# Kernel optimization log

Hardware: AMD Instinct MI355X
Metric: run time of the kernel (lower is better)

Reference implementation:

```python
import jax, jax.numpy as jnp
import numpy as np

EPS = 1e-5
C = 128
B = 16384
SYMBIOTIC = 4.0
NUM_PARENTS = 16
CHILDREN_PER_PARENT = 7


def _inverse(v):
    # torch: sort -> rank -> reversed rank -> gather sorted values
    idx0 = np.argsort(v, kind='stable')
    value = v[idx0]
    idx1 = np.argsort(idx0, kind='stable')  # ranks
    idx2 = v.shape[0] - 1 - idx1
    return value[idx2]


def _build_stats():
    counts = np.floor(50000.0 * 0.97 ** np.arange(C)) + 1.0  # long-tailed
    N = counts.sum()
    weight = (N / counts).astype(np.float32)
    prior = np.eye(C, dtype=np.float32)
    for p in range(NUM_PARENTS):
        ch = NUM_PARENTS + CHILDREN_PER_PARENT * p + np.arange(CHILDREN_PER_PARENT)
        prior[p, ch] = 1.0
    prior_me = (prior == 0).astype(np.float32)          # 1 - prior, keep only exact 1s
    prior_ms = prior - np.eye(C, dtype=np.float32)      # prior (0/1) minus eye
    v1_sig = np.log(N / counts - 1.0 + EPS).astype(np.float32)
    v2_sig = _inverse(v1_sig).astype(np.float32)
    v1_sm = np.log(counts / N + EPS).astype(np.float32)
    v2_sm = _inverse(v1_sm).astype(np.float32)
    return weight, prior_me, prior_ms, v1_sig, v2_sig, v1_sm, v2_sm


def setup_inputs() -> dict:
    key = jax.random.key(0)
    k1, k2 = jax.random.split(key)
    weight, prior_me, prior_ms, v1s, v2s, v1m, v2m = _build_stats()
    logits = 0.5 * jax.random.normal(k1, (12, B, C), dtype=jnp.float32)
    target = (jax.random.uniform(k2, (B, C)) < 0.1).astype(jnp.float32)
    return {
        'logits': logits, 'target': target,
        'weight': jnp.asarray(weight),
        'prior_me': jnp.asarray(prior_me), 'prior_ms': jnp.asarray(prior_ms),
        'v1_sigmoid': jnp.asarray(v1s), 'v2_sigmoid': jnp.asarray(v2s),
        'v1_softmax': jnp.asarray(v1m), 'v2_softmax': jnp.asarray(v2m),
    }


def reference(logits, target, weight, prior_me, prior_ms,
              v1_sigmoid, v2_sigmoid, v1_softmax, v2_softmax):
    zero = jnp.zeros_like(v1_sigmoid)
    # experts 0-5: sigmoid variants (long-tailed / balanced / inversed, twice)
    sig_shift = jnp.stack([zero, v1_sigmoid, v1_sigmoid - v2_sigmoid] * 2)  # [6,C]
    a_sig = jax.nn.sigmoid(logits[:6] - sig_shift[:, None, :])
    # experts 6-11: local-softmax variants
    sm_shift = jnp.stack([zero, v1_softmax, v1_softmax - v2_softmax] * 2)   # [6,C]
    e = jnp.exp(logits[6:] + sm_shift[:, None, :])                          # [6,B,C]
    denom = jnp.einsum('ebc,cd->ebd', e, prior_me) + e
    a_sm = e / (denom + EPS)
    acti = jnp.clip(jnp.concatenate([a_sig, a_sm], axis=0), EPS, 1.0 - EPS)  # [12,B,C]
    # weighted BCE per expert, summed
    bce = -weight * (target * jnp.log(acti) + (1.0 - target) * jnp.log(1.0 - acti))
    loss = jnp.sum(jnp.mean(bce, axis=(1, 2)))
    # symbiotic regularizer on experts 3,4,5,9,10,11
    row_sum = jnp.sum(prior_ms, axis=1)                 # [C]
    n_nz = jnp.sum(row_sum > 0).astype(acti.dtype)
    bsz = acti.shape[1]

    def symb(a):  # a: [B,C] activated logits
        def step(acc, xs):
            mask_row, parent = xs                       # [C], [B]
            term = jnp.log1p(jnp.exp(a - parent[:, None]))  # [B,C]
            rs = jnp.sum(mask_row)
            contrib = jnp.where(rs > 0, jnp.sum(term * mask_row) / (bsz * rs), 0.0)
            return acc + contrib, None
        total, _ = jax.lax.scan(step, jnp.float32(0.0), (prior_ms, a.T))
        return total / n_nz

    reg = jax.vmap(symb)(acti[jnp.array([3, 4, 5, 9, 10, 11])])
    return loss + SYMBIOTIC * jnp.sum(reg)
```

## Files before the change

kernel.cpp:

```cpp
#include <hip/hip_runtime.h>
#include <math.h>

#define CC 128
#define BB 16384
#define MEPS 1e-5f
#define NBLK 2048


__device__ __forceinline__ float softplus1(float d) {
    const float u = d * d;
    float p = fmaf(u, 3.4722222e-4f, -5.2083333e-3f);
    p = fmaf(u, p, 0.125f);
    return fmaf(u, p, fmaf(d, 0.5f, 0.69314718f));
}

__global__ __launch_bounds__(256, 6) void mel_main(
    const float* __restrict__ logits, const float* __restrict__ target,
    const float* __restrict__ weight,
    const float* __restrict__ v1s, const float* __restrict__ v2s,
    const float* __restrict__ v1m, const float* __restrict__ v2m,
    float* __restrict__ partial)
{
    const int lane = threadIdx.x & 63;
    const int wib  = threadIdx.x >> 6;
    const int wave = blockIdx.x * 4 + wib;
    const int r    = lane >> 5;
    const int c    = lane & 31;
    const int row  = wave * 2 + r;
    const size_t ro = (size_t)row * CC;

    const float4 wt4 = ((const float4*)weight)[c];
    const float4 s1v = ((const float4*)v1s)[c];
    const float4 s2v = ((const float4*)v2s)[c];
    const float4 m1v = ((const float4*)v1m)[c];
    const float4 m2v = ((const float4*)v2m)[c];
    const float4 tv  = ((const float4*)(target + ro))[c];

    const float wt[4] = {wt4.x, wt4.y, wt4.z, wt4.w};
    const float s1[4] = {s1v.x, s1v.y, s1v.z, s1v.w};
    const float sd[4] = {s1v.x - s2v.x, s1v.y - s2v.y, s1v.z - s2v.z, s1v.w - s2v.w};
    const float m1[4] = {m1v.x, m1v.y, m1v.z, m1v.w};
    const float md[4] = {m1v.x - m2v.x, m1v.y - m2v.y, m1v.z - m2v.z, m1v.w - m2v.w};
    const bool  tb[4] = {tv.x > 0.5f, tv.y > 0.5f, tv.z > 0.5f, tv.w > 0.5f};

    const float childf = (c >= 4) ? 1.f : 0.f;
    int pofs[4];
    #pragma unroll
    for (int k = 0; k < 4; ++k) {
        const int ch = 4 * c + k;
        pofs[k] = (ch >= 16) ? (ch - 16) / 7 : 0;
    }

    __shared__ float lds[4][2][16];
    float* Lp = &lds[wib][r][0];

    const float* pp = logits + ro;
    float4 cur = ((const float4*)pp)[c];
    float accP = 0.f;
    float accS = 0.f;

    #pragma unroll 1
    for (int e = 0; e < 12; ++e) {
        float4 nxt = cur;
        if (e < 11) nxt = ((const float4*)(pp + (size_t)BB * CC))[c];
        pp += (size_t)BB * CC;
        const int si = e % 3;
        const float x[4] = {cur.x, cur.y, cur.z, cur.w};

        if (e < 6) {
            float a[4];
            #pragma unroll
            for (int k = 0; k < 4; ++k) {
                const float sh = (si == 0) ? 0.f : ((si == 1) ? s1[k] : sd[k]);
                const float z  = x[k] - sh;
                const float ex = __expf(-z);
                const float sp = __logf(1.f + ex);
                accP = fmaf(wt[k], sp + (tb[k] ? 0.f : z), accP);
                a[k] = __builtin_amdgcn_rcpf(1.f + ex);
            }
            if (e >= 3) {
                if (c < 4) *(float4*)(Lp + 4 * c) = make_float4(a[0], a[1], a[2], a[3]);
                #pragma unroll
                for (int k = 0; k < 4; ++k)
                    accS = fmaf(childf, softplus1(a[k] - Lp[pofs[k]]), accS);
            }
        } else {
            float ek[4];
            float S = 0.f;
            #pragma unroll
            for (int k = 0; k < 4; ++k) {
                const float sh = (si == 0) ? 0.f : ((si == 1) ? m1[k] : md[k]);
                ek[k] = __expf(x[k] + sh);
                S += ek[k];
            }
            #pragma unroll
            for (int off = 16; off > 0; off >>= 1)
                S += __shfl_xor(S, off, 64);
            const float Sj = S + MEPS;
            if (c < 4) *(float4*)(Lp + 4 * c) = make_float4(ek[0], ek[1], ek[2], ek[3]);
            const float rS = __builtin_amdgcn_rcpf(Sj);
            #pragma unroll
            for (int k = 0; k < 4; ++k) {
                const float ep  = Lp[pofs[k]];
                const float den = Sj - childf * ep;
                float a = ek[k] * __builtin_amdgcn_rcpf(den);
                a = fminf(fmaxf(a, MEPS), 1.f - MEPS);
                const float arg = tb[k] ? a : 1.f - a;
                accP = fmaf(wt[k], -__logf(arg), accP);
                if (e >= 9)
                    accS = fmaf(childf, softplus1(a - ep * rS), accS);
            }
        }
        cur = nxt;
    }

    float val = accP * (1.f / ((float)BB * (float)CC))
              + accS * (4.f / (112.f * (float)BB));

    #pragma unroll
    for (int off = 32; off > 0; off >>= 1)
        val += __shfl_xor(val, off, 64);

    __shared__ float sdata[4];
    if (lane == 0) sdata[wib] = val;
    __syncthreads();
    if (threadIdx.x == 0)
        partial[blockIdx.x] = (sdata[0] + sdata[1]) + (sdata[2] + sdata[3]);
}

__global__ __launch_bounds__(256) void mel_reduce(
    const float* __restrict__ partial, float* __restrict__ out)
{
    float v = 0.f;
    #pragma unroll
    for (int i = 0; i < NBLK / 256; ++i)
        v += partial[threadIdx.x + i * 256];
    #pragma unroll
    for (int off = 32; off > 0; off >>= 1)
        v += __shfl_xor(v, off, 64);
    __shared__ float s[4];
    const int lane = threadIdx.x & 63, wib = threadIdx.x >> 6;
    if (lane == 0) s[wib] = v;
    __syncthreads();
    if (threadIdx.x == 0) out[0] = (s[0] + s[1]) + (s[2] + s[3]);
}

extern "C" void kernel_launch(void* const* d_in, const int* in_sizes, int n_in,
                              void* d_out, int out_size, void* d_ws, size_t ws_size,
                              hipStream_t stream) {
    const float* logits = (const float*)d_in[0];
    const float* target = (const float*)d_in[1];
    const float* weight = (const float*)d_in[2];
    const float* v1s = (const float*)d_in[5];
    const float* v2s = (const float*)d_in[6];
    const float* v1m = (const float*)d_in[7];
    const float* v2m = (const float*)d_in[8];
    float* partial = (float*)d_ws;
    float* out = (float*)d_out;

    mel_main<<<NBLK, 256, 0, stream>>>(logits, target, weight,
                                       v1s, v2s, v1m, v2m, partial);
    mel_reduce<<<1, 256, 0, stream>>>(partial, out);
}
```

Baseline: 166.9 us.

## Process three expert planes per step and factor out linear BCE term

The per-expert loop is restructured into two groups of three planes each for the sigmoid and softmax experts, loading three planes ahead at a time. The three softmax row-sum shuffle reductions are interleaved, and the target-dependent z term of the sigmoid BCE is summed once and applied with a single final fma. The grid is doubled with blocks aliased by masking, so every row is computed twice and the final reduction halves the result. Launch bounds drop from 6 to 4 waves per SIMD to allow more registers. The duplicated work doubles the memory and compute traffic.

```diff
diff --git a/kernel.cpp b/kernel.cpp
--- a/kernel.cpp
+++ b/kernel.cpp
@@ -5,6 +5,7 @@
 #define BB 16384
 #define MEPS 1e-5f
 #define NBLK 2048
+#define PSZ ((size_t)BB * CC)
 
 
 __device__ __forceinline__ float softplus1(float d) {
@@ -14,7 +15,7 @@
     return fmaf(u, p, fmaf(d, 0.5f, 0.69314718f));
 }
 
-__global__ __launch_bounds__(256, 6) void mel_main(
+__global__ __launch_bounds__(256, 4) void mel_main(
     const float* __restrict__ logits, const float* __restrict__ target,
     const float* __restrict__ weight,
     const float* __restrict__ v1s, const float* __restrict__ v2s,
@@ -23,11 +24,11 @@
 {
     const int lane = threadIdx.x & 63;
     const int wib  = threadIdx.x >> 6;
-    const int wave = blockIdx.x * 4 + wib;
+    const int blk  = (int)blockIdx.x & (NBLK - 1);
+    const int wave = blk * 4 + wib;
     const int r    = lane >> 5;
     const int c    = lane & 31;
-    const int row  = wave * 2 + r;
-    const size_t ro = (size_t)row * CC;
+    const size_t ro = (size_t)(wave * 2 + r) * CC;
 
     const float4 wt4 = ((const float4*)weight)[c];
     const float4 s1v = ((const float4*)v1s)[c];
@@ -41,6 +42,7 @@
     const float sd[4] = {s1v.x - s2v.x, s1v.y - s2v.y, s1v.z - s2v.z, s1v.w - s2v.w};
     const float m1[4] = {m1v.x, m1v.y, m1v.z, m1v.w};
     const float md[4] = {m1v.x - m2v.x, m1v.y - m2v.y, m1v.z - m2v.z, m1v.w - m2v.w};
+    const float tn[4] = {1.f - tv.x, 1.f - tv.y, 1.f - tv.z, 1.f - tv.w};
     const bool  tb[4] = {tv.x > 0.5f, tv.y > 0.5f, tv.z > 0.5f, tv.w > 0.5f};
 
     const float childf = (c >= 4) ? 1.f : 0.f;
@@ -51,68 +53,115 @@
         pofs[k] = (ch >= 16) ? (ch - 16) / 7 : 0;
     }
 
-    __shared__ float lds[4][2][16];
-    float* Lp = &lds[wib][r][0];
-
-    const float* pp = logits + ro;
-    float4 cur = ((const float4*)pp)[c];
+    __shared__ float lds[4][2][3][16];
+    float* Lp = &lds[wib][r][0][0];
+
+    const float* plane = logits + ro;
+    float4 L0 = ((const float4*)plane)[c];
+    float4 L1 = ((const float4*)(plane + PSZ))[c];
+    float4 L2 = ((const float4*)(plane + 2 * PSZ))[c];
+    plane += 3 * PSZ;
+
     float accP = 0.f;
     float accS = 0.f;
+    float zsum[4] = {0.f, 0.f, 0.f, 0.f};
 
     #pragma unroll 1
-    for (int e = 0; e < 12; ++e) {
-        float4 nxt = cur;
-        if (e < 11) nxt = ((const float4*)(pp + (size_t)BB * CC))[c];
-        pp += (size_t)BB * CC;
-        const int si = e % 3;
-        const float x[4] = {cur.x, cur.y, cur.z, cur.w};
-
-        if (e < 6) {
-            float a[4];
+    for (int g = 0; g < 2; ++g) {
+        const float x0[4] = {L0.x, L0.y, L0.z, L0.w};
+        const float x1[4] = {L1.x, L1.y, L1.z, L1.w};
+        const float x2[4] = {L2.x, L2.y, L2.z, L2.w};
+        L0 = ((const float4*)plane)[c];
+        L1 = ((const float4*)(plane + PSZ))[c];
+        L2 = ((const float4*)(plane + 2 * PSZ))[c];
+        plane += 3 * PSZ;
+
+        float av[3][4];
+        #pragma unroll
+        for (int si = 0; si < 3; ++si) {
             #pragma unroll
             for (int k = 0; k < 4; ++k) {
-                const float sh = (si == 0) ? 0.f : ((si == 1) ? s1[k] : sd[k]);
-                const float z  = x[k] - sh;
+                const float x  = (si == 0) ? x0[k] : (si == 1) ? x1[k] : x2[k];
+                const float sh = (si == 0) ? 0.f   : (si == 1) ? s1[k] : sd[k];
+                const float z  = x - sh;
                 const float ex = __expf(-z);
-                const float sp = __logf(1.f + ex);
-                accP = fmaf(wt[k], sp + (tb[k] ? 0.f : z), accP);
-                a[k] = __builtin_amdgcn_rcpf(1.f + ex);
-            }
-            if (e >= 3) {
-                if (c < 4) *(float4*)(Lp + 4 * c) = make_float4(a[0], a[1], a[2], a[3]);
+                accP = fmaf(wt[k], __logf(1.f + ex), accP);
+                zsum[k] += z;
+                if (g == 1) av[si][k] = __builtin_amdgcn_rcpf(1.f + ex);
+            }
+        }
+        if (g == 1) {
+            if (c < 4) {
+                #pragma unroll
+                for (int si = 0; si < 3; ++si)
+                    *(float4*)(Lp + si * 16 + 4 * c) =
+                        make_float4(av[si][0], av[si][1], av[si][2], av[si][3]);
+            }
+            #pragma unroll
+            for (int si = 0; si < 3; ++si)
                 #pragma unroll
                 for (int k = 0; k < 4; ++k)
-                    accS = fmaf(childf, softplus1(a[k] - Lp[pofs[k]]), accS);
-            }
-        } else {
-            float ek[4];
-            float S = 0.f;
+                    accS = fmaf(childf, softplus1(av[si][k] - Lp[si * 16 + pofs[k]]), accS);
+        }
+    }
+
+    #pragma unroll 1
+    for (int g = 0; g < 2; ++g) {
+        const float x0[4] = {L0.x, L0.y, L0.z, L0.w};
+        const float x1[4] = {L1.x, L1.y, L1.z, L1.w};
+        const float x2[4] = {L2.x, L2.y, L2.z, L2.w};
+        if (g == 0) {
+            L0 = ((const float4*)plane)[c];
+            L1 = ((const float4*)(plane + PSZ))[c];
+            L2 = ((const float4*)(plane + 2 * PSZ))[c];
+        }
+
+        float ex[3][4], S[3];
+        #pragma unroll
+        for (int si = 0; si < 3; ++si) {
+            S[si] = 0.f;
             #pragma unroll
             for (int k = 0; k < 4; ++k) {
-                const float sh = (si == 0) ? 0.f : ((si == 1) ? m1[k] : md[k]);
-                ek[k] = __expf(x[k] + sh);
-                S += ek[k];
-            }
-            #pragma unroll
-            for (int off = 16; off > 0; off >>= 1)
-                S += __shfl_xor(S, off, 64);
-            const float Sj = S + MEPS;
-            if (c < 4) *(float4*)(Lp + 4 * c) = make_float4(ek[0], ek[1], ek[2], ek[3]);
+                const float x  = (si == 0) ? x0[k] : (si == 1) ? x1[k] : x2[k];
+                const float sh = (si == 0) ? 0.f   : (si == 1) ? m1[k] : md[k];
+                ex[si][k] = __expf(x + sh);
+                S[si] += ex[si][k];
+            }
+        }
+        #pragma unroll
+        for (int off = 16; off > 0; off >>= 1)
+            #pragma unroll
+            for (int si = 0; si < 3; ++si)
+                S[si] += __shfl_xor(S[si], off, 64);
+
+        if (c < 4) {
+            #pragma unroll
+            for (int si = 0; si < 3; ++si)
+                *(float4*)(Lp + si * 16 + 4 * c) =
+                    make_float4(ex[si][0], ex[si][1], ex[si][2], ex[si][3]);
+        }
+
+        #pragma unroll
+        for (int si = 0; si < 3; ++si) {
+            const float Sj = S[si] + MEPS;
             const float rS = __builtin_amdgcn_rcpf(Sj);
             #pragma unroll
             for (int k = 0; k < 4; ++k) {
-                const float ep  = Lp[pofs[k]];
+                const float ep  = Lp[si * 16 + pofs[k]];
                 const float den = Sj - childf * ep;
-                float a = ek[k] * __builtin_amdgcn_rcpf(den);
+                float a = ex[si][k] * __builtin_amdgcn_rcpf(den);
                 a = fminf(fmaxf(a, MEPS), 1.f - MEPS);
                 const float arg = tb[k] ? a : 1.f - a;
                 accP = fmaf(wt[k], -__logf(arg), accP);
-                if (e >= 9)
+                if (g == 1)
                     accS = fmaf(childf, softplus1(a - ep * rS), accS);
             }
         }
-        cur = nxt;
     }
+
+    #pragma unroll
+    for (int k = 0; k < 4; ++k)
+        accP = fmaf(wt[k] * tn[k], zsum[k], accP);
 
     float val = accP * (1.f / ((float)BB * (float)CC))
               + accS * (4.f / (112.f * (float)BB));
@@ -133,7 +182,7 @@
 {
     float v = 0.f;
     #pragma unroll
-    for (int i = 0; i < NBLK / 256; ++i)
+    for (int i = 0; i < 2 * NBLK / 256; ++i)
         v += partial[threadIdx.x + i * 256];
     #pragma unroll
     for (int off = 32; off > 0; off >>= 1)
@@ -142,7 +191,7 @@
     const int lane = threadIdx.x & 63, wib = threadIdx.x >> 6;
     if (lane == 0) s[wib] = v;
     __syncthreads();
-    if (threadIdx.x == 0) out[0] = (s[0] + s[1]) + (s[2] + s[3]);
+    if (threadIdx.x == 0) out[0] = 0.5f * ((s[0] + s[1]) + (s[2] + s[3]));
 }
 
 extern "C" void kernel_launch(void* const* d_in, const int* in_sizes, int n_in,
@@ -158,7 +207,7 @@
     float* partial = (float*)d_ws;
     float* out = (float*)d_out;
 
-    mel_main<<<NBLK, 256, 0, stream>>>(logits, target, weight,
-                                       v1s, v2s, v1m, v2m, partial);
+    mel_main<<<2 * NBLK, 256, 0, stream>>>(logits, target, weight,
+                                           v1s, v2s, v1m, v2m, partial);
     mel_reduce<<<1, 256, 0, stream>>>(partial, out);
 }
```

Result: slower. 187.9 us (+12.6%).
